# Optimization experiments

Measured on AMD Instinct MI355X. Metric: run time of the kernel, lower is better.

## Reference

```python
import jax, jax.numpy as jnp
import numpy as np

D = 64          # lrp_out_dim
L = 16          # lrp_length
LEN_SEQ = 4     # int(sqrt(L))
N = 200000      # nodes
E = 800000      # edges
NPERM = 250000  # permutation patterns
P = NPERM * L   # perm slots (sparse matrix rows)
G = 4096        # graphs (pooling output rows)


def _spmm(row, col, val, m, dense):
    # sparse [m, n] @ dense [n, d] via gather + segment_sum
    return jax.ops.segment_sum(val[:, None] * dense[col], row, num_segments=m)


def setup_inputs() -> dict:
    key = jax.random.key(0)
    ks = jax.random.split(key, 16)
    x = jax.random.normal(ks[0], (N, D), jnp.float32)
    efeat = jax.random.normal(ks[1], (E, D), jnp.float32)
    degs = jax.random.uniform(ks[2], (N,), jnp.float32) * 8.0
    n2p_row = jax.random.randint(ks[3], (P,), 0, P)
    n2p_col = jax.random.randint(ks[4], (P,), 0, N)
    n2p_val = jax.random.uniform(ks[5], (P,), jnp.float32)
    e2p_row = jax.random.randint(ks[6], (P,), 0, P)
    e2p_col = jax.random.randint(ks[7], (P,), 0, E)
    e2p_val = jax.random.uniform(ks[8], (P,), jnp.float32)
    pool_row = jax.random.randint(ks[9], (NPERM,), 0, G)
    pool_col = jax.random.randint(ks[10], (NPERM,), 0, NPERM)
    pool_val = jnp.ones((NPERM,), jnp.float32)
    weights = jax.random.normal(ks[11], (D, D, L), jnp.float32)
    bias = jnp.zeros((1, D), jnp.float32)
    W0 = jax.random.normal(ks[12], (2 * D, LEN_SEQ), jnp.float32) * 0.1
    b0 = jnp.zeros((2 * D,), jnp.float32)
    W1 = jax.random.normal(ks[13], (D, 2 * D), jnp.float32) * 0.1
    b1 = jnp.zeros((D,), jnp.float32)
    Wl = jax.random.normal(ks[14], (D, D), jnp.float32) * 0.1
    bl = jnp.zeros((D,), jnp.float32)
    return dict(x=x, efeat=efeat, degs=degs,
                n2p_row=n2p_row, n2p_col=n2p_col, n2p_val=n2p_val,
                e2p_row=e2p_row, e2p_col=e2p_col, e2p_val=e2p_val,
                pool_row=pool_row, pool_col=pool_col, pool_val=pool_val,
                weights=weights, bias=bias, W0=W0, b0=b0, W1=W1, b1=b1,
                Wl=Wl, bl=bl)


def reference(x, efeat, degs,
              n2p_row, n2p_col, n2p_val,
              e2p_row, e2p_col, e2p_val,
              pool_row, pool_col, pool_val,
              weights, bias, W0, b0, W1, b1, Wl, bl):
    # permutation gather of node and edge features into perm slots: [P, D]
    nfeat = _spmm(n2p_row, n2p_col, n2p_val, P, x) \
          + _spmm(e2p_row, e2p_col, e2p_val, P, efeat)
    deg_perm = _spmm(n2p_row, n2p_col, n2p_val, P, degs[:, None])  # [P, 1]
    # transpose->view->permute in torch is equivalent to a plain reshape here
    nfeat = nfeat.reshape(NPERM, L, D)           # [n_perms, L, D]
    # diagonal-position degree entries: columns 0, 5, 10, 15
    deg_perm = deg_perm.reshape(NPERM, L)[:, jnp.arange(0, L, LEN_SEQ + 1)]  # [n_perms, 4]
    # einsum 'dab,bca->dc' with nfeat [n, a=L, b=D], weights [b=D, c=D, a=L]
    h = jnp.einsum('nlb,bcl->nc', nfeat, weights) + bias
    h = jax.nn.relu(h) @ Wl.T + bl               # self.linear(relu(...))
    dg = jax.nn.relu(deg_perm @ W0.T + b0) @ W1.T + b1  # degree MLP gate
    out = h * dg                                  # [n_perms, D]
    return _spmm(pool_row, pool_col, pool_val, G, out)  # [G, D]
```

## Files before the change

### kernel.cpp

```cpp
#include <hip/hip_runtime.h>

#define NPERM_C 250000
#define P_C     4000000
#define G_C     4096
#define NB1     1954
#define NB2     123

typedef __attribute__((ext_vector_type(8))) short bf16x8;
typedef __attribute__((ext_vector_type(4))) float f32x4;

static __device__ __forceinline__ unsigned short f2bf(float f) {
    unsigned u = __float_as_uint(f);
    unsigned r = (u + 0x7fffu + ((u >> 16) & 1u)) >> 16;
    return (unsigned short)r;
}
static __device__ __forceinline__ float bf2f(unsigned short s) {
    return __uint_as_float(((unsigned)s) << 16);
}
static __device__ __forceinline__ unsigned long long pack4(ushort4 s) {
    return (unsigned long long)s.x | ((unsigned long long)s.y << 16) |
           ((unsigned long long)s.z << 32) | ((unsigned long long)s.w << 48);
}

__global__ void repack_bpk(const float* __restrict__ w, unsigned short* __restrict__ bpk) {
    int o = blockIdx.x * 256 + threadIdx.x;
    int j = o & 7, lane = (o >> 3) & 63, h = (o >> 9) & 1;
    int nt = (o >> 10) & 3, ks = (o >> 12) & 1, l = o >> 13;
    int b = ks * 32 + (lane >> 4) * 8 + j;
    int c = nt * 16 + (lane & 15);
    float wv = w[(b * 64 + c) * 16 + l];
    unsigned short hb = f2bf(wv);
    bpk[o] = (h == 0) ? hb : f2bf(wv - bf2f(hb));
}

__global__ void repack_wlpk(const float* __restrict__ wl, unsigned short* __restrict__ wpk) {
    int o = blockIdx.x * 256 + threadIdx.x;
    int j = o & 7, lane = (o >> 3) & 63, h = (o >> 9) & 1;
    int nt = (o >> 10) & 3, ks = o >> 12;
    int k = ks * 32 + (lane >> 4) * 8 + j;
    int c2 = nt * 16 + (lane & 15);
    float wv = wl[c2 * 64 + k];
    unsigned short hb = f2bf(wv);
    wpk[o] = (h == 0) ? hb : f2bf(wv - bf2f(hb));
}

__global__ __launch_bounds__(256) void pool_hist(const int* __restrict__ pcol,
                                                 int* __restrict__ poolCnt) {
    int i = blockIdx.x * 256 + threadIdx.x;
    if (i < NPERM_C) atomicAdd(&poolCnt[pcol[i]], 1);
}

__global__ __launch_bounds__(256) void pool_scan_local(const int* __restrict__ poolCnt,
                                                       int* __restrict__ poolRk,
                                                       int* __restrict__ bsum2) {
    __shared__ int ts[256];
    int b = blockIdx.x, t = threadIdx.x;
    int base = b * 2048 + t * 8;
    int v[8]; int s = 0;
#pragma unroll
    for (int i = 0; i < 8; ++i) {
        int idx = base + i;
        v[i] = (idx < NPERM_C) ? (poolCnt[idx] != 0) : 0;
        s += v[i];
    }
    ts[t] = s;
    __syncthreads();
    for (int ofs = 1; ofs < 256; ofs <<= 1) {
        int xv = (t >= ofs) ? ts[t - ofs] : 0;
        __syncthreads();
        ts[t] += xv;
        __syncthreads();
    }
    int run = ts[t] - s;
    if (t == 255) bsum2[b] = ts[255];
#pragma unroll
    for (int i = 0; i < 8; ++i) {
        int idx = base + i;
        if (idx < NPERM_C) poolRk[idx] = run;
        run += v[i];
    }
}

__global__ void pool_scan_top(int* __restrict__ bsum2) {
    __shared__ int ts[256];
    int t = threadIdx.x;
    int v = (t < NB2) ? bsum2[t] : 0;
    ts[t] = v;
    __syncthreads();
    for (int ofs = 1; ofs < 256; ofs <<= 1) {
        int xv = (t >= ofs) ? ts[t - ofs] : 0;
        __syncthreads();
        ts[t] += xv;
        __syncthreads();
    }
    if (t < NB2) bsum2[t] = ts[t] - v;
}

__global__ __launch_bounds__(256) void pool_scan_add(const int* __restrict__ poolCnt,
                                                     int* __restrict__ poolRk,
                                                     const int* __restrict__ bsum2,
                                                     int* __restrict__ nActB) {
    int b = blockIdx.x, t = threadIdx.x;
    int add = bsum2[b];
    int base = b * 2048 + t * 8;
#pragma unroll
    for (int i = 0; i < 8; ++i) {
        int idx = base + i;
        if (idx < NPERM_C) {
            int flag = poolCnt[idx] != 0;
            int o = poolRk[idx] + add;
            poolRk[idx] = (o << 1) | flag;
            if (idx == NPERM_C - 1) nActB[0] = o + flag;
        }
    }
}

__global__ __launch_bounds__(256) void hist(const int* __restrict__ r1,
                                            const int* __restrict__ r2,
                                            const int* __restrict__ poolRk,
                                            int* __restrict__ cnt) {
    int i8 = (blockIdx.x * 256 + threadIdx.x) * 8;
    if (i8 >= 2 * P_C) return;
    const int* src = (i8 < P_C) ? (r1 + i8) : (r2 + (i8 - P_C));
    int4 ra = *reinterpret_cast<const int4*>(src);
    int4 rb = *reinterpret_cast<const int4*>(src + 4);
    int rr[8] = {ra.x, ra.y, ra.z, ra.w, rb.x, rb.y, rb.z, rb.w};
#pragma unroll
    for (int q = 0; q < 8; ++q) {
        int info = poolRk[rr[q] >> 4];
        if (info & 1) atomicAdd(&cnt[(info >> 1) * 16 + (rr[q] & 15)], 1);
    }
}

__global__ __launch_bounds__(256) void scan_local(const int* __restrict__ cnt,
                                                  int* __restrict__ off,
                                                  int* __restrict__ bsum) {
    __shared__ int ts[256];
    int b = blockIdx.x, t = threadIdx.x;
    int base = b * 2048 + t * 8;
    int v[8]; int s = 0;
#pragma unroll
    for (int i = 0; i < 8; ++i) {
        int idx = base + i;
        v[i] = (idx < P_C) ? cnt[idx] : 0;
        s += v[i];
    }
    ts[t] = s;
    __syncthreads();
    for (int ofs = 1; ofs < 256; ofs <<= 1) {
        int xv = (t >= ofs) ? ts[t - ofs] : 0;
        __syncthreads();
        ts[t] += xv;
        __syncthreads();
    }
    int run = ts[t] - s;
    if (t == 255) bsum[b] = ts[255];
#pragma unroll
    for (int i = 0; i < 8; ++i) {
        int idx = base + i;
        if (idx < P_C) off[idx] = run;
        run += v[i];
    }
}

__global__ void scan_top(int* __restrict__ bsum) {
    __shared__ int ts[256];
    int t = threadIdx.x;
    int base = t * 8;
    int v[8]; int s = 0;
#pragma unroll
    for (int i = 0; i < 8; ++i) {
        int idx = base + i;
        v[i] = (idx < NB1) ? bsum[idx] : 0;
        s += v[i];
    }
    ts[t] = s;
    __syncthreads();
    for (int ofs = 1; ofs < 256; ofs <<= 1) {
        int xv = (t >= ofs) ? ts[t - ofs] : 0;
        __syncthreads();
        ts[t] += xv;
        __syncthreads();
    }
    int run = ts[t] - s;
#pragma unroll
    for (int i = 0; i < 8; ++i) {
        int idx = base + i;
        if (idx < NB1) bsum[idx] = run;
        run += v[i];
    }
}

__global__ __launch_bounds__(256) void scan_add(int* __restrict__ off,
                                                const int* __restrict__ bsum,
                                                int* __restrict__ cur) {
    int b = blockIdx.x, t = threadIdx.x;
    int add = bsum[b];
    int base = b * 2048 + t * 8;
#pragma unroll
    for (int i = 0; i < 8; ++i) {
        int idx = base + i;
        if (idx < P_C) {
            int o = off[idx] + add;
            if (idx == P_C - 1) off[P_C] = o + cur[idx];
            off[idx] = o;
            cur[idx] = o;
        }
    }
}

__global__ __launch_bounds__(256) void scat(
        const int* __restrict__ r1, const int* __restrict__ c1, const float* __restrict__ v1,
        const int* __restrict__ r2, const int* __restrict__ c2, const float* __restrict__ v2,
        const int* __restrict__ poolRk,
        int* __restrict__ cur, unsigned long long* __restrict__ suv) {
    int i2 = (blockIdx.x * 256 + threadIdx.x) * 2;
    if (i2 >= 2 * P_C) return;
    const int* rr; const int* cc; const float* vv; unsigned srcbit; int base;
    if (i2 < P_C) { rr = r1; cc = c1; vv = v1; srcbit = 0u; base = i2; }
    else          { rr = r2; cc = c2; vv = v2; srcbit = 0x100000u; base = i2 - P_C; }
    int2 r = *reinterpret_cast<const int2*>(rr + base);
    int2 c = *reinterpret_cast<const int2*>(cc + base);
    float2 v = *reinterpret_cast<const float2*>(vv + base);
    {
        int info = poolRk[r.x >> 4];
        if (info & 1) {
            int pos = atomicAdd(&cur[(info >> 1) * 16 + (r.x & 15)], 1);
            unsigned long long e = (unsigned long long)((unsigned)c.x | srcbit) |
                                   ((unsigned long long)__float_as_uint(v.x) << 32);
            __builtin_nontemporal_store(e, suv + pos);
        }
    }
    {
        int info = poolRk[r.y >> 4];
        if (info & 1) {
            int pos = atomicAdd(&cur[(info >> 1) * 16 + (r.y & 15)], 1);
            unsigned long long e = (unsigned long long)((unsigned)c.y | srcbit) |
                                   ((unsigned long long)__float_as_uint(v.y) << 32);
            __builtin_nontemporal_store(e, suv + pos);
        }
    }
}

#define PROC(kv, acc, isdg)  do { \
    unsigned k_ = (unsigned)(kv); float v_ = __uint_as_float((unsigned)((kv) >> 32)); \
    const float* f_ = (k_ & 0x100000u) ? efeat : x; \
    float4 fv_ = *reinterpret_cast<const float4*>(f_ + (size_t)(k_ & 0xFFFFFu) * 64 + t16 * 4); \
    acc.x = fmaf(v_, fv_.x, acc.x); acc.y = fmaf(v_, fv_.y, acc.y); \
    acc.z = fmaf(v_, fv_.z, acc.z); acc.w = fmaf(v_, fv_.w, acc.w); \
    if ((isdg) && !(k_ & 0x100000u)) dq = fmaf(v_, degs[k_ & 0xFFFFFu], dq); \
} while (0)

__global__ __launch_bounds__(256) void gather_nfeat(
        const unsigned long long* __restrict__ suv, const int* __restrict__ pOff,
        const float* __restrict__ x, const float* __restrict__ efeat,
        const float* __restrict__ degs, const int* __restrict__ nActB,
        unsigned short* __restrict__ nfH, unsigned short* __restrict__ nfL,
        float* __restrict__ degD, int row0, int rows) {
    int nAct = nActB[0];
    int t = threadIdx.x;
    int gid = t >> 4;
    int t16 = t & 15;
    int r4 = gid >> 2;
    int q4 = gid & 3;
    int cr = row0 + blockIdx.x * 4 + r4;
    int rend = row0 + rows; if (rend > nAct) rend = nAct;
    if (cr >= rend) return;
    int sBase = cr * 16 + q4 * 4;
    int4 bo = *reinterpret_cast<const int4*>(pOff + sBase);
    int e4 = pOff[sBase + 4];
    int i0 = bo.x, e0 = bo.y;
    int i1 = bo.y, e1 = bo.z;
    int i2 = bo.z, e2 = bo.w;
    int i3 = bo.w, e3 = e4;
    float4 a0 = {0,0,0,0}, a1 = {0,0,0,0}, a2 = {0,0,0,0}, a3 = {0,0,0,0};
    float dq = 0.f;
    while ((i0 < e0) | (i1 < e1) | (i2 < e2) | (i3 < e3)) {
        bool h0 = i0 < e0, h1 = i1 < e1, h2 = i2 < e2, h3 = i3 < e3;
        bool g0 = i0 + 1 < e0, g1 = i1 + 1 < e1, g2 = i2 + 1 < e2, g3 = i3 + 1 < e3;
        unsigned long long ka0, kb0, ka1, kb1, ka2, kb2, ka3, kb3;
        if (h0) ka0 = __builtin_nontemporal_load(suv + i0);
        if (g0) kb0 = __builtin_nontemporal_load(suv + i0 + 1);
        if (h1) ka1 = __builtin_nontemporal_load(suv + i1);
        if (g1) kb1 = __builtin_nontemporal_load(suv + i1 + 1);
        if (h2) ka2 = __builtin_nontemporal_load(suv + i2);
        if (g2) kb2 = __builtin_nontemporal_load(suv + i2 + 1);
        if (h3) ka3 = __builtin_nontemporal_load(suv + i3);
        if (g3) kb3 = __builtin_nontemporal_load(suv + i3 + 1);
        if (h0) PROC(ka0, a0, q4 == 0);
        if (g0) PROC(kb0, a0, q4 == 0);
        if (h1) PROC(ka1, a1, q4 == 1);
        if (g1) PROC(kb1, a1, q4 == 1);
        if (h2) PROC(ka2, a2, q4 == 2);
        if (g2) PROC(kb2, a2, q4 == 2);
        if (h3) PROC(ka3, a3, q4 == 3);
        if (g3) PROC(kb3, a3, q4 == 3);
        i0 += 2; i1 += 2; i2 += 2; i3 += 2;
    }
    size_t o = ((size_t)(cr - row0) * 16 + q4 * 4) * 64 + t16 * 4;
    float4 as[4] = {a0, a1, a2, a3};
#pragma unroll
    for (int c = 0; c < 4; ++c) {
        ushort4 h4, l4;
        h4.x = f2bf(as[c].x); l4.x = f2bf(as[c].x - bf2f(h4.x));
        h4.y = f2bf(as[c].y); l4.y = f2bf(as[c].y - bf2f(h4.y));
        h4.z = f2bf(as[c].z); l4.z = f2bf(as[c].z - bf2f(h4.z));
        h4.w = f2bf(as[c].w); l4.w = f2bf(as[c].w - bf2f(h4.w));
        __builtin_nontemporal_store(pack4(h4),
            reinterpret_cast<unsigned long long*>(nfH + o + (size_t)c * 64));
        __builtin_nontemporal_store(pack4(l4),
            reinterpret_cast<unsigned long long*>(nfL + o + (size_t)c * 64));
    }
    if (t16 == 0) degD[(size_t)cr * 4 + q4] = dq;
}

__global__ __launch_bounds__(256) void dg_gemm(
        const float* __restrict__ degD,
        const float* __restrict__ W0, const float* __restrict__ b0,
        const float* __restrict__ W1, const float* __restrict__ b1,
        const int* __restrict__ nActB,
        float* __restrict__ dgb, int r0, int rows) {
    __shared__ float hidT[128][68];
    __shared__ float w1T[128][68];
    __shared__ float dloc[64][4];
    __shared__ float w0s[128][5];
    int nAct = nActB[0];
    int rend = r0 + rows; if (rend > nAct) rend = nAct;
    int t = threadIdx.x;
    int m0 = r0 + blockIdx.x * 64;
    if (m0 >= rend) return;

    {
        int r = t >> 2, j = t & 3;
        int gr = m0 + r; if (gr >= rend) gr = rend - 1;
        dloc[r][j] = degD[(size_t)gr * 4 + j];
    }
    if (t < 128) {
        w0s[t][0] = W0[t * 4 + 0]; w0s[t][1] = W0[t * 4 + 1];
        w0s[t][2] = W0[t * 4 + 2]; w0s[t][3] = W0[t * 4 + 3];
        w0s[t][4] = b0[t];
    }
    for (int s = 0; s < 32; ++s) {
        int idx = t + s * 256;
        w1T[idx & 127][idx >> 7] = W1[idx];
    }
    __syncthreads();
    for (int s = 0; s < 32; ++s) {
        int idx = t + s * 256;
        int h = idx & 127, r = idx >> 7;
        float v = w0s[h][4] + dloc[r][0] * w0s[h][0] + dloc[r][1] * w0s[h][1]
                            + dloc[r][2] * w0s[h][2] + dloc[r][3] * w0s[h][3];
        hidT[h][r] = fmaxf(v, 0.f);
    }
    __syncthreads();

    int tm = t >> 4, tn = t & 15;
    float acc[4][4] = {};
#pragma unroll 8
    for (int k = 0; k < 128; ++k) {
        float4 a = *reinterpret_cast<const float4*>(&hidT[k][tm * 4]);
        float4 b = *reinterpret_cast<const float4*>(&w1T[k][tn * 4]);
        acc[0][0] = fmaf(a.x, b.x, acc[0][0]); acc[0][1] = fmaf(a.x, b.y, acc[0][1]);
        acc[0][2] = fmaf(a.x, b.z, acc[0][2]); acc[0][3] = fmaf(a.x, b.w, acc[0][3]);
        acc[1][0] = fmaf(a.y, b.x, acc[1][0]); acc[1][1] = fmaf(a.y, b.y, acc[1][1]);
        acc[1][2] = fmaf(a.y, b.z, acc[1][2]); acc[1][3] = fmaf(a.y, b.w, acc[1][3]);
        acc[2][0] = fmaf(a.z, b.x, acc[2][0]); acc[2][1] = fmaf(a.z, b.y, acc[2][1]);
        acc[2][2] = fmaf(a.z, b.z, acc[2][2]); acc[2][3] = fmaf(a.z, b.w, acc[2][3]);
        acc[3][0] = fmaf(a.w, b.x, acc[3][0]); acc[3][1] = fmaf(a.w, b.y, acc[3][1]);
        acc[3][2] = fmaf(a.w, b.z, acc[3][2]); acc[3][3] = fmaf(a.w, b.w, acc[3][3]);
    }
    float bb[4] = {b1[tn * 4 + 0], b1[tn * 4 + 1], b1[tn * 4 + 2], b1[tn * 4 + 3]};
#pragma unroll
    for (int i = 0; i < 4; ++i) {
        int grow = m0 + tm * 4 + i;
        if (grow < rend) {
            float4 o = {acc[i][0] + bb[0], acc[i][1] + bb[1],
                        acc[i][2] + bb[2], acc[i][3] + bb[3]};
            *reinterpret_cast<float4*>(&dgb[(size_t)grow * 64 + tn * 4]) = o;
        }
    }
}

__global__ __launch_bounds__(256) void gemm_mfma(
        const unsigned short* __restrict__ nfH, const unsigned short* __restrict__ nfL,
        const unsigned short* __restrict__ Bpk, const unsigned short* __restrict__ Wlpk,
        const float* __restrict__ bias, const float* __restrict__ bl,
        const float* __restrict__ dgb, const int* __restrict__ nActB,
        float* __restrict__ outb, int r0, int rows) {
    __shared__ unsigned short Hh[128][72];
    __shared__ unsigned short Hl[128][72];
    int nAct = nActB[0];
    int rowsEff = rows; if (r0 + rowsEff > nAct) rowsEff = nAct - r0;
    int t = threadIdx.x, lane = t & 63, w = t >> 6;
    int m0 = blockIdx.x * 128;
    if (m0 >= rowsEff) return;
    int r16 = lane & 15, kg = lane >> 4;

    f32x4 acc[2][4];
#pragma unroll
    for (int i = 0; i < 2; ++i)
#pragma unroll
        for (int j = 0; j < 4; ++j) acc[i][j] = (f32x4){0.f, 0.f, 0.f, 0.f};

    for (int l = 0; l < 16; ++l) {
#pragma unroll
        for (int ks = 0; ks < 2; ++ks) {
            bf16x8 ah[2], al[2];
#pragma unroll
            for (int mt = 0; mt < 2; ++mt) {
                int lr = m0 + w * 32 + mt * 16 + r16;
                if (lr >= rowsEff) lr = rowsEff - 1;
                size_t off = ((size_t)lr * 16 + l) * 64 + ks * 32 + kg * 8;
                ah[mt] = *reinterpret_cast<const bf16x8*>(nfH + off);
                al[mt] = *reinterpret_cast<const bf16x8*>(nfL + off);
            }
#pragma unroll
            for (int nt = 0; nt < 4; ++nt) {
                const unsigned short* bb =
                    Bpk + (size_t)(((l * 2 + ks) * 4 + nt) * 2) * 512 + lane * 8;
                bf16x8 bh = *reinterpret_cast<const bf16x8*>(bb);
                bf16x8 blo = *reinterpret_cast<const bf16x8*>(bb + 512);
#pragma unroll
                for (int mt = 0; mt < 2; ++mt) {
                    acc[mt][nt] = __builtin_amdgcn_mfma_f32_16x16x32_bf16(ah[mt], bh,  acc[mt][nt], 0, 0, 0);
                    acc[mt][nt] = __builtin_amdgcn_mfma_f32_16x16x32_bf16(ah[mt], blo, acc[mt][nt], 0, 0, 0);
                    acc[mt][nt] = __builtin_amdgcn_mfma_f32_16x16x32_bf16(al[mt], bh,  acc[mt][nt], 0, 0, 0);
                }
            }
        }
    }

#pragma unroll
    for (int mt = 0; mt < 2; ++mt)
#pragma unroll
        for (int nt = 0; nt < 4; ++nt) {
            int col = nt * 16 + r16;
            float bv = bias[col];
#pragma unroll
            for (int reg = 0; reg < 4; ++reg) {
                int rl = w * 32 + mt * 16 + kg * 4 + reg;
                float h = fmaxf(acc[mt][nt][reg] + bv, 0.f);
                unsigned short hb = f2bf(h);
                Hh[rl][col] = hb;
                Hl[rl][col] = f2bf(h - bf2f(hb));
            }
        }
    __syncthreads();

    f32x4 acc2[2][4];
#pragma unroll
    for (int i = 0; i < 2; ++i)
#pragma unroll
        for (int j = 0; j < 4; ++j) acc2[i][j] = (f32x4){0.f, 0.f, 0.f, 0.f};

#pragma unroll
    for (int ks = 0; ks < 2; ++ks) {
        bf16x8 ah[2], al[2];
#pragma unroll
        for (int mt = 0; mt < 2; ++mt) {
            int rl = w * 32 + mt * 16 + r16;
            ah[mt] = *reinterpret_cast<const bf16x8*>(&Hh[rl][ks * 32 + kg * 8]);
            al[mt] = *reinterpret_cast<const bf16x8*>(&Hl[rl][ks * 32 + kg * 8]);
        }
#pragma unroll
        for (int nt = 0; nt < 4; ++nt) {
            const unsigned short* wb =
                Wlpk + (size_t)(((ks * 4 + nt) * 2)) * 512 + lane * 8;
            bf16x8 bh = *reinterpret_cast<const bf16x8*>(wb);
            bf16x8 blo = *reinterpret_cast<const bf16x8*>(wb + 512);
#pragma unroll
            for (int mt = 0; mt < 2; ++mt) {
                acc2[mt][nt] = __builtin_amdgcn_mfma_f32_16x16x32_bf16(ah[mt], bh,  acc2[mt][nt], 0, 0, 0);
                acc2[mt][nt] = __builtin_amdgcn_mfma_f32_16x16x32_bf16(ah[mt], blo, acc2[mt][nt], 0, 0, 0);
                acc2[mt][nt] = __builtin_amdgcn_mfma_f32_16x16x32_bf16(al[mt], bh,  acc2[mt][nt], 0, 0, 0);
            }
        }
    }

#pragma unroll
    for (int mt = 0; mt < 2; ++mt)
#pragma unroll
        for (int nt = 0; nt < 4; ++nt) {
            int col = nt * 16 + r16;
            float bv = bl[col];
#pragma unroll
            for (int reg = 0; reg < 4; ++reg) {
                int rl = w * 32 + mt * 16 + kg * 4 + reg;
                if (m0 + rl < rowsEff) {
                    size_t idx = (size_t)(r0 + m0 + rl) * 64 + col;
                    outb[idx] = (acc2[mt][nt][reg] + bv) * dgb[idx];
                }
            }
        }
}

__global__ __launch_bounds__(256) void pool_scatter(
        const int* __restrict__ prow, const int* __restrict__ pcol,
        const float* __restrict__ pval, const int* __restrict__ poolRk,
        const float* __restrict__ outb, float* __restrict__ out) {
    int t = blockIdx.x * 256 + threadIdx.x;
    int i = t >> 6, d = t & 63;
    if (i >= NPERM_C) return;
    int r = prow[i], c = pcol[i];
    float v = pval[i];
    int cr = poolRk[c] >> 1;
    atomicAdd(&out[(size_t)r * 64 + d], v * outb[(size_t)cr * 64 + d]);
}

extern "C" void kernel_launch(void* const* d_in, const int* in_sizes, int n_in,
                              void* d_out, int out_size, void* d_ws, size_t ws_size,
                              hipStream_t stream) {
    const float* x       = (const float*)d_in[0];
    const float* efeat   = (const float*)d_in[1];
    const float* degs    = (const float*)d_in[2];
    const int*   n2p_row = (const int*)d_in[3];
    const int*   n2p_col = (const int*)d_in[4];
    const float* n2p_val = (const float*)d_in[5];
    const int*   e2p_row = (const int*)d_in[6];
    const int*   e2p_col = (const int*)d_in[7];
    const float* e2p_val = (const float*)d_in[8];
    const int*   pool_row = (const int*)d_in[9];
    const int*   pool_col = (const int*)d_in[10];
    const float* pool_val = (const float*)d_in[11];
    const float* weights = (const float*)d_in[12];
    const float* bias    = (const float*)d_in[13];
    const float* W0      = (const float*)d_in[14];
    const float* b0      = (const float*)d_in[15];
    const float* W1      = (const float*)d_in[16];
    const float* b1      = (const float*)d_in[17];
    const float* Wl      = (const float*)d_in[18];
    const float* bl      = (const float*)d_in[19];
    float* out = (float*)d_out;

    unsigned long long* suv = (unsigned long long*)d_ws;
    int*   pOff     = (int*)(suv + 8000000);
    int*   pCur     = pOff + 4000064;
    int*   bsum     = pCur + 4000000;
    int*   poolCnt  = bsum + 2048;
    int*   poolRk   = poolCnt + 250000;
    int*   bsum2    = poolRk + 250000;
    int*   nActB    = bsum2 + 256;
    unsigned short* Bpk  = (unsigned short*)(nActB + 16);
    unsigned short* Wlpk = Bpk + 131072;
    float* degD = (float*)(Wlpk + 8192);
    float* dgb  = degD + 1000000;
    float* outb = dgb;
    unsigned short* nfH = (unsigned short*)(dgb + 16000000);

    const long long base_elems = 16000000LL + 4000064 + 4000000 + 2048 +
                                 250000 * 2 + 256 + 16 + 65536 + 4096 +
                                 1000000 + 16000000;
    long long availf = (long long)(ws_size / 4) - base_elems;
    long long chl = availf / 1024;
    if (chl > NPERM_C) chl = NPERM_C;
    int CH = (int)(chl & ~127LL);
    if (CH < 128) {
        hipMemsetAsync(d_out, 0, (size_t)out_size * 4, stream);
        return;
    }
    unsigned short* nfL = nfH + (size_t)CH * 1024;

    hipMemsetAsync(pCur, 0, (size_t)P_C * 4, stream);
    hipMemsetAsync(poolCnt, 0, (size_t)NPERM_C * 4, stream);
    hipMemsetAsync(out, 0, (size_t)G_C * 64 * 4, stream);

    repack_bpk<<<512, 256, 0, stream>>>(weights, Bpk);
    repack_wlpk<<<32, 256, 0, stream>>>(Wl, Wlpk);

    pool_hist<<<(NPERM_C + 255) / 256, 256, 0, stream>>>(pool_col, poolCnt);
    pool_scan_local<<<NB2, 256, 0, stream>>>(poolCnt, poolRk, bsum2);
    pool_scan_top<<<1, 256, 0, stream>>>(bsum2);
    pool_scan_add<<<NB2, 256, 0, stream>>>(poolCnt, poolRk, bsum2, nActB);

    hist<<<3907, 256, 0, stream>>>(n2p_row, e2p_row, poolRk, pCur);
    scan_local<<<NB1, 256, 0, stream>>>(pCur, pOff, bsum);
    scan_top<<<1, 256, 0, stream>>>(bsum);
    scan_add<<<NB1, 256, 0, stream>>>(pOff, bsum, pCur);
    scat<<<15625, 256, 0, stream>>>(n2p_row, n2p_col, n2p_val,
                                    e2p_row, e2p_col, e2p_val,
                                    poolRk, pCur, suv);

    for (int c0 = 0; c0 < NPERM_C; c0 += CH) {
        int rows = NPERM_C - c0; if (rows > CH) rows = CH;
        gather_nfeat<<<(rows + 3) / 4, 256, 0, stream>>>(
            suv, pOff, x, efeat, degs, nActB, nfH, nfL, degD, c0, rows);
        dg_gemm<<<(rows + 63) / 64, 256, 0, stream>>>(
            degD, W0, b0, W1, b1, nActB, dgb, c0, rows);
        gemm_mfma<<<(rows + 127) / 128, 256, 0, stream>>>(
            nfH, nfL, Bpk, Wlpk, bias, bl, dgb, nActB, outb, c0, rows);
    }

    pool_scatter<<<62500, 256, 0, stream>>>(pool_row, pool_col, pool_val,
                                            poolRk, outb, out);
}
```

Baseline: 1.348 ms.

## Replace atomic pooling scatter with CSR-by-row gather

Builds a CSR grouping of pooling entries by output graph row (histogram, single-block scan, scatter of (compact row, value) pairs), then replaces the atomic-add scatter of 16M float atomics with a per-row gather that accumulates in registers and writes each output once. This removes heavy atomic contention on the 4096x64 output and the output memset. It adds three small kernels and a 2MB entry buffer, and the gather has uneven per-row work of about 61 entries on average.

```diff
diff --git a/kernel.cpp b/kernel.cpp
--- a/kernel.cpp
+++ b/kernel.cpp
@@ -44,10 +44,15 @@
     wpk[o] = (h == 0) ? hb : f2bf(wv - bf2f(hb));
 }
 
-__global__ __launch_bounds__(256) void pool_hist(const int* __restrict__ pcol,
-                                                 int* __restrict__ poolCnt) {
+__global__ __launch_bounds__(256) void pool_hist2(const int* __restrict__ pcol,
+                                                  const int* __restrict__ prow,
+                                                  int* __restrict__ poolCnt,
+                                                  int* __restrict__ rowCnt) {
     int i = blockIdx.x * 256 + threadIdx.x;
-    if (i < NPERM_C) atomicAdd(&poolCnt[pcol[i]], 1);
+    if (i < NPERM_C) {
+        atomicAdd(&poolCnt[pcol[i]], 1);
+        atomicAdd(&rowCnt[prow[i]], 1);
+    }
 }
 
 __global__ __launch_bounds__(256) void pool_scan_local(const int* __restrict__ poolCnt,
@@ -113,6 +118,44 @@
             if (idx == NPERM_C - 1) nActB[0] = o + flag;
         }
     }
+}
+
+__global__ void row_scan(const int* __restrict__ rowCnt,
+                         int* __restrict__ rowOff, int* __restrict__ rowCur) {
+    __shared__ int ts[256];
+    int t = threadIdx.x;
+    int base = t * 16;
+    int v[16]; int s = 0;
+#pragma unroll
+    for (int i = 0; i < 16; ++i) { v[i] = rowCnt[base + i]; s += v[i]; }
+    ts[t] = s;
+    __syncthreads();
+    for (int ofs = 1; ofs < 256; ofs <<= 1) {
+        int xv = (t >= ofs) ? ts[t - ofs] : 0;
+        __syncthreads();
+        ts[t] += xv;
+        __syncthreads();
+    }
+    int run = ts[t] - s;
+#pragma unroll
+    for (int i = 0; i < 16; ++i) {
+        rowOff[base + i] = run;
+        rowCur[base + i] = run;
+        run += v[i];
+    }
+    if (t == 255) rowOff[G_C] = run;
+}
+
+__global__ __launch_bounds__(256) void pool_scat(
+        const int* __restrict__ prow, const int* __restrict__ pcol,
+        const float* __restrict__ pval, const int* __restrict__ poolRk,
+        int* __restrict__ rowCur, uint2* __restrict__ pent) {
+    int i = blockIdx.x * 256 + threadIdx.x;
+    if (i >= NPERM_C) return;
+    int r = prow[i];
+    int cr = poolRk[pcol[i]] >> 1;
+    int pos = atomicAdd(&rowCur[r], 1);
+    pent[pos] = make_uint2((unsigned)cr, __float_as_uint(pval[i]));
 }
 
 __global__ __launch_bounds__(256) void hist(const int* __restrict__ r1,
@@ -494,17 +537,28 @@
         }
 }
 
-__global__ __launch_bounds__(256) void pool_scatter(
-        const int* __restrict__ prow, const int* __restrict__ pcol,
-        const float* __restrict__ pval, const int* __restrict__ poolRk,
+__global__ __launch_bounds__(256) void pool_gather(
+        const uint2* __restrict__ pent, const int* __restrict__ rowOff,
         const float* __restrict__ outb, float* __restrict__ out) {
-    int t = blockIdx.x * 256 + threadIdx.x;
-    int i = t >> 6, d = t & 63;
-    if (i >= NPERM_C) return;
-    int r = prow[i], c = pcol[i];
-    float v = pval[i];
-    int cr = poolRk[c] >> 1;
-    atomicAdd(&out[(size_t)r * 64 + d], v * outb[(size_t)cr * 64 + d]);
+    int t = threadIdx.x;
+    int w = t >> 6, d = t & 63;
+    int r = blockIdx.x * 4 + w;
+    int b0 = rowOff[r], b1 = rowOff[r + 1];
+    float acc = 0.f;
+    int e = b0;
+    for (; e + 1 < b1; e += 2) {
+        uint2 p0 = pent[e];
+        uint2 p1 = pent[e + 1];
+        float v0 = __uint_as_float(p0.y);
+        float v1 = __uint_as_float(p1.y);
+        acc = fmaf(v0, outb[(size_t)p0.x * 64 + d], acc);
+        acc = fmaf(v1, outb[(size_t)p1.x * 64 + d], acc);
+    }
+    if (e < b1) {
+        uint2 p0 = pent[e];
+        acc = fmaf(__uint_as_float(p0.y), outb[(size_t)p0.x * 64 + d], acc);
+    }
+    out[(size_t)r * 64 + d] = acc;
 }
 
 extern "C" void kernel_launch(void* const* d_in, const int* in_sizes, int n_in,
@@ -540,7 +594,11 @@
     int*   poolRk   = poolCnt + 250000;
     int*   bsum2    = poolRk + 250000;
     int*   nActB    = bsum2 + 256;
-    unsigned short* Bpk  = (unsigned short*)(nActB + 16);
+    int*   rowCnt   = nActB + 16;
+    int*   rowOff   = rowCnt + 4096;
+    int*   rowCur   = rowOff + 4160;
+    uint2* pent     = (uint2*)(rowCur + 4096);
+    unsigned short* Bpk  = (unsigned short*)(pent + 250000);
     unsigned short* Wlpk = Bpk + 131072;
     float* degD = (float*)(Wlpk + 8192);
     float* dgb  = degD + 1000000;
@@ -548,7 +606,8 @@
     unsigned short* nfH = (unsigned short*)(dgb + 16000000);
 
     const long long base_elems = 16000000LL + 4000064 + 4000000 + 2048 +
-                                 250000 * 2 + 256 + 16 + 65536 + 4096 +
+                                 250000 * 2 + 256 + 16 + 4096 + 4160 + 4096 +
+                                 500000 + 65536 + 4096 +
                                  1000000 + 16000000;
     long long availf = (long long)(ws_size / 4) - base_elems;
     long long chl = availf / 1024;
@@ -562,15 +621,20 @@
 
     hipMemsetAsync(pCur, 0, (size_t)P_C * 4, stream);
     hipMemsetAsync(poolCnt, 0, (size_t)NPERM_C * 4, stream);
-    hipMemsetAsync(out, 0, (size_t)G_C * 64 * 4, stream);
+    hipMemsetAsync(rowCnt, 0, (size_t)G_C * 4, stream);
 
     repack_bpk<<<512, 256, 0, stream>>>(weights, Bpk);
     repack_wlpk<<<32, 256, 0, stream>>>(Wl, Wlpk);
 
-    pool_hist<<<(NPERM_C + 255) / 256, 256, 0, stream>>>(pool_col, poolCnt);
+    pool_hist2<<<(NPERM_C + 255) / 256, 256, 0, stream>>>(pool_col, pool_row,
+                                                          poolCnt, rowCnt);
     pool_scan_local<<<NB2, 256, 0, stream>>>(poolCnt, poolRk, bsum2);
     pool_scan_top<<<1, 256, 0, stream>>>(bsum2);
     pool_scan_add<<<NB2, 256, 0, stream>>>(poolCnt, poolRk, bsum2, nActB);
+    row_scan<<<1, 256, 0, stream>>>(rowCnt, rowOff, rowCur);
+    pool_scat<<<(NPERM_C + 255) / 256, 256, 0, stream>>>(pool_row, pool_col,
+                                                         pool_val, poolRk,
+                                                         rowCur, pent);
 
     hist<<<3907, 256, 0, stream>>>(n2p_row, e2p_row, poolRk, pCur);
     scan_local<<<NB1, 256, 0, stream>>>(pCur, pOff, bsum);
@@ -590,6 +654,5 @@
             nfH, nfL, Bpk, Wlpk, bias, bl, dgb, nActB, outb, c0, rows);
     }
 
-    pool_scatter<<<62500, 256, 0, stream>>>(pool_row, pool_col, pool_val,
-                                            poolRk, outb, out);
-}
+    pool_gather<<<1024, 256, 0, stream>>>(pent, rowOff, outb, out);
+}
```

New measurement: 1.360 ms. About the same (+0.9%).
